# Kernel tuning notes

Hardware: AMD Instinct MI355X
Metric: run time of the kernel (lower is better)

Reference implementation:

```python
import jax, jax.numpy as jnp
import numpy as np
import math

MODEL_DIM = 1024
NUM_HEADS = 16
ATTN_DIM = MODEL_DIM // NUM_HEADS  # 64
ROWS, COLS, AXES = 32, 32, 2
PAIRS = ATTN_DIM // (AXES * 2)     # 16
BATCH = 4
TOKENS = ROWS * COLS               # 1024


def setup_inputs() -> dict:
    key = jax.random.key(0)
    ks = jax.random.split(key, 8)
    s = 1.0 / math.sqrt(MODEL_DIM)
    return {
        "x": jax.random.normal(ks[0], (BATCH, TOKENS, MODEL_DIM), jnp.float32),
        "cos": jax.random.uniform(ks[1], (ROWS, COLS, AXES, PAIRS), jnp.float32),
        "sin": jax.random.uniform(ks[2], (ROWS, COLS, AXES, PAIRS), jnp.float32),
        "Wq": jax.random.normal(ks[3], (MODEL_DIM, MODEL_DIM), jnp.float32) * s,
        "Wk": jax.random.normal(ks[4], (MODEL_DIM, MODEL_DIM), jnp.float32) * s,
        "Wv": jax.random.normal(ks[5], (MODEL_DIM, MODEL_DIM), jnp.float32) * s,
        "Wo": jax.random.normal(ks[6], (MODEL_DIM, MODEL_DIM), jnp.float32) * s,
        "bo": jax.random.normal(ks[7], (MODEL_DIM,), jnp.float32) * 0.01,
    }


def _apply_rope(W, cos, sin):
    # W: (b, h, tokens, attn_dim) -> (b, h, rows, cols, axes, pairs, 2)
    b, h, n, d = W.shape
    rows, cols, axes, pairs = cos.shape
    Wp = W.reshape(b, h, rows, cols, axes, pairs, 2)
    c = cos[None, None]
    s = sin[None, None]
    w0, w1 = Wp[..., 0], Wp[..., 1]
    out = jnp.stack([c * w0 - s * w1, s * w0 + c * w1], axis=-1)
    return out.reshape(b, h, n, d)


def reference(x, cos, sin, Wq, Wk, Wv, Wo, bo):
    b, n, _ = x.shape
    # torch Linear: y = x @ W.T
    Q = (x @ Wq.T).reshape(b, n, NUM_HEADS, ATTN_DIM).transpose(0, 2, 1, 3)
    K = (x @ Wk.T).reshape(b, n, NUM_HEADS, ATTN_DIM).transpose(0, 2, 1, 3)
    V = (x @ Wv.T).reshape(b, n, NUM_HEADS, ATTN_DIM).transpose(0, 2, 1, 3)
    Q = _apply_rope(Q, cos, sin)
    K = _apply_rope(K, cos, sin)
    scores = jnp.einsum("bhqd,bhkd->bhqk", Q, K) / math.sqrt(ATTN_DIM)
    attn = jax.nn.softmax(scores, axis=-1)
    o = jnp.einsum("bhqk,bhkd->bhqd", attn, V)
    o = o.transpose(0, 2, 1, 3).reshape(b, n, MODEL_DIM)
    return o @ Wo.T + bo
```

## Files before the change

kernel.cpp:

```cpp
#include <hip/hip_runtime.h>
#include <hip/hip_bf16.h>

typedef __bf16 bf16;
typedef __bf16 bf16x4 __attribute__((ext_vector_type(4)));
typedef __bf16 bf16x8 __attribute__((ext_vector_type(8)));
typedef float  f32x4  __attribute__((ext_vector_type(4)));
typedef unsigned int u32x2 __attribute__((ext_vector_type(2)));

#define MFMA16(a, b, c) __builtin_amdgcn_mfma_f32_16x16x32_bf16((a), (b), (c), 0, 0, 0)

#define GLOBAL_AS(p) ((const __attribute__((address_space(1))) void*)(p))
#define LDS_AS(p)    ((__attribute__((address_space(3))) void*)(p))

#define BATCH 4
#define TOK   1024
#define DIM   1024
#define HEADS 16
#define HD    64
#define MTOT  (BATCH * TOK)
#define MELEM (1024u * 1024u)

__global__ __launch_bounds__(256) void k_prep(
    const float* __restrict__ X,
    const float* __restrict__ W0, const float* __restrict__ W1,
    const float* __restrict__ W2, const float* __restrict__ W3,
    bf16* __restrict__ xh, bf16* __restrict__ wsp)
{
    const int bid = blockIdx.x;
    if (bid < 2048) {
        size_t i0 = ((size_t)bid * 256 + threadIdx.x) * 8;
        f32x4 a = *(const f32x4*)(X + i0);
        f32x4 b = *(const f32x4*)(X + i0 + 4);
        bf16x8 h;
        #pragma unroll
        for (int j = 0; j < 4; j++) { h[j] = (bf16)a[j]; h[4 + j] = (bf16)b[j]; }
        *(bf16x8*)(xh + i0) = h;
    } else {
        const int b2 = bid - 2048;
        const int widx = b2 >> 9;
        const int inner = b2 & 511;
        const float* W = (widx == 0) ? W0 : (widx == 1) ? W1 : (widx == 2) ? W2 : W3;
        size_t i0 = ((size_t)inner * 256 + threadIdx.x) * 8;
        f32x4 a = *(const f32x4*)(W + i0);
        f32x4 b = *(const f32x4*)(W + i0 + 4);
        bf16x8 h, l;
        #pragma unroll
        for (int j = 0; j < 4; j++) {
            bf16 g0 = (bf16)a[j]; h[j] = g0;     l[j] = (bf16)(a[j] - (float)g0);
            bf16 g1 = (bf16)b[j]; h[4 + j] = g1; l[4 + j] = (bf16)(b[j] - (float)g1);
        }
        *(bf16x8*)(wsp + (size_t)widx * MELEM + i0) = h;
        if (widx == 3)
            *(bf16x8*)(wsp + 4 * (size_t)MELEM + i0) = l;
    }
}

__global__ __launch_bounds__(512) void k_gemmQKV(
    const bf16* __restrict__ Ag, const bf16* __restrict__ wsp,
    const float* __restrict__ cosT, const float* __restrict__ sinT,
    bf16* __restrict__ q_o, bf16* __restrict__ k_o, bf16* __restrict__ v_o)
{
    __shared__ bf16 lds[24576];
    bf16* A0 = lds;
    bf16* A1 = lds + 4096;
    bf16* B0 = lds + 8192;
    bf16* B1 = lds + 16384;

    const int fid = blockIdx.x;
    const int swz = (fid & 7) * 48 + (fid >> 3);
    const int nt = swz % 12;
    const int mt = swz / 12;

    const int t = threadIdx.x;
    const int lane = t & 63;
    const int w = t >> 6;
    const int wr = w >> 2, wc = w & 3;
    const int l15 = lane & 15;
    const int grp = lane >> 4;

    f32x4 acc[4][4];
    #pragma unroll
    for (int m = 0; m < 4; m++)
        #pragma unroll
        for (int n = 0; n < 4; n++)
            #pragma unroll
            for (int r = 0; r < 4; r++) acc[m][n][r] = 0.f;

    const int srow = lane >> 2;
    const int schk8 = ((lane & 3) ^ ((lane >> 3) & 3)) * 8;
    const bf16* asrc = Ag  + (size_t)(mt * 128 + srow) * DIM + schk8;
    const bf16* bsrc = wsp + (size_t)(nt * 256 + srow) * DIM + schk8;

    auto stage = [&](int k, bf16* ab, bf16* bb) {
        const int k0 = k * 32;
        __builtin_amdgcn_global_load_lds(
            GLOBAL_AS(asrc + (size_t)w * 16 * DIM + k0),
            LDS_AS(ab + w * 512), 16, 0, 0);
        #pragma unroll
        for (int jj = 0; jj < 2; ++jj) {
            int j = w * 2 + jj;
            __builtin_amdgcn_global_load_lds(
                GLOBAL_AS(bsrc + (size_t)j * 16 * DIM + k0),
                LDS_AS(bb + j * 512), 16, 0, 0);
        }
    };

    auto compute = [&](const bf16* ab, const bf16* bb) {
        bf16x8 fb[4];
        #pragma unroll
        for (int n = 0; n < 4; n++) {
            int rb = wc * 64 + n * 16 + l15;
            fb[n] = *(const bf16x8*)&bb[rb * 32 + ((grp ^ ((rb >> 1) & 3)) << 3)];
        }
        __builtin_amdgcn_s_setprio(1);
        #pragma unroll
        for (int m = 0; m < 4; m++) {
            int r = wr * 64 + m * 16 + l15;
            bf16x8 fa = *(const bf16x8*)&ab[r * 32 + ((grp ^ ((r >> 1) & 3)) << 3)];
            #pragma unroll
            for (int n = 0; n < 4; n++)
                acc[m][n] = MFMA16(fa, fb[n], acc[m][n]);
        }
        __builtin_amdgcn_s_setprio(0);
    };

    stage(0, A0, B0);
    #pragma unroll 1
    for (int kk = 0; kk < 16; kk++) {
        __syncthreads();
        stage(2 * kk + 1, A1, B1);
        compute(A0, B0);
        __syncthreads();
        if (kk < 15) stage(2 * kk + 2, A0, B0);
        compute(A1, B1);
    }

    const int mode = nt >> 2;
    const int h = (nt & 3) * 4 + wc;
    if (mode == 2) {
        #pragma unroll
        for (int m = 0; m < 4; m++) {
            const int grow0 = mt * 128 + wr * 64 + m * 16 + grp * 4;
            const int b = grow0 >> 10, ntok0 = grow0 & (TOK - 1);
            #pragma unroll
            for (int n = 0; n < 4; n++) {
                const int d = n * 16 + l15;
                bf16x4 pk;
                #pragma unroll
                for (int r = 0; r < 4; r++) pk[r] = (bf16)acc[m][n][r];
                *(bf16x4*)&v_o[((size_t)((b * HEADS + h) * HD + d)) * TOK + ntok0] = pk;
            }
        }
    } else {
        __syncthreads();
        float* cosL = (float*)lds;
        float* sinL = (float*)(lds + 8192);
        const int tb = (mt & 7) * 128;
        *(f32x4*)(cosL + t * 8)     = *(const f32x4*)(cosT + (size_t)tb * 32 + t * 8);
        *(f32x4*)(cosL + t * 8 + 4) = *(const f32x4*)(cosT + (size_t)tb * 32 + t * 8 + 4);
        *(f32x4*)(sinL + t * 8)     = *(const f32x4*)(sinT + (size_t)tb * 32 + t * 8);
        *(f32x4*)(sinL + t * 8 + 4) = *(const f32x4*)(sinT + (size_t)tb * 32 + t * 8 + 4);
        __syncthreads();

        bf16* dst = (mode == 0) ? q_o : k_o;
        const float sc = (mode == 0) ? 0.18033688f : 1.0f;
        #pragma unroll
        for (int m = 0; m < 4; m++) {
            const int grow0 = mt * 128 + wr * 64 + m * 16 + grp * 4;
            const int b = grow0 >> 10, ntok0 = grow0 & (TOK - 1);
            const int loc0 = wr * 64 + m * 16 + grp * 4;
            #pragma unroll
            for (int n = 0; n < 4; n++) {
                const int d = n * 16 + l15;
                const int idp = (d >> 5) * 16 + ((d >> 1) & 15);
                const bool ev = (d & 1) == 0;
                #pragma unroll
                for (int r = 0; r < 4; r++) {
                    float v = acc[m][n][r];
                    float pr = __shfl_xor(v, 1, 64);
                    float c = cosL[(loc0 + r) * 32 + idp];
                    float s = sinL[(loc0 + r) * 32 + idp];
                    float res = (ev ? (c * v - s * pr) : (s * pr + c * v)) * sc;
                    dst[((size_t)(b * HEADS + h) * TOK + ntok0 + r) * HD + d] = (bf16)res;
                }
            }
        }
    }
}

__global__ __launch_bounds__(256) void k_gemmO(
    const bf16* __restrict__ Ag, const bf16* __restrict__ wsp,
    const float* __restrict__ bo, float* __restrict__ f_o)
{
    __shared__ bf16 Alin[64 * 64];
    __shared__ bf16 Bhlin[128 * 64];
    __shared__ bf16 Bllin[128 * 64];

    const bf16* Bh_g = wsp + 3 * (size_t)MELEM;
    const bf16* Bl_g = wsp + 4 * (size_t)MELEM;

    const int fid = blockIdx.x;
    const int swz = (fid & 7) * 64 + (fid >> 3);
    const int nt = swz & 7;
    const int mt = swz >> 3;

    const int t = threadIdx.x;
    const int lane = t & 63;
    const int w = t >> 6;
    const int wr = w >> 1, wc = w & 1;
    const int l15 = lane & 15;

    f32x4 acc[2][4];
    #pragma unroll
    for (int m = 0; m < 2; m++)
        #pragma unroll
        for (int n = 0; n < 4; n++)
            #pragma unroll
            for (int r = 0; r < 4; r++) acc[m][n][r] = 0.f;

    const int srow = lane >> 3;
    const int schk8 = ((lane & 7) ^ (srow & 7)) * 8;
    const bf16* asrc  = Ag   + (size_t)(mt * 64 + srow) * DIM + schk8;
    const bf16* bhsrc = Bh_g + (size_t)(nt * 128 + srow) * DIM + schk8;
    const bf16* blsrc = Bl_g + (size_t)(nt * 128 + srow) * DIM + schk8;

    for (int k0 = 0; k0 < DIM; k0 += 64) {
        __syncthreads();
        #pragma unroll
        for (int ii = 0; ii < 2; ++ii) {
            int i = w * 2 + ii;
            __builtin_amdgcn_global_load_lds(
                GLOBAL_AS(asrc + (size_t)i * 8 * DIM + k0),
                LDS_AS(&Alin[i * 512]), 16, 0, 0);
        }
        #pragma unroll
        for (int jj = 0; jj < 4; ++jj) {
            int j = w * 4 + jj;
            size_t roff = (size_t)j * 8 * DIM + k0;
            __builtin_amdgcn_global_load_lds(GLOBAL_AS(bhsrc + roff),
                                             LDS_AS(&Bhlin[j * 512]), 16, 0, 0);
            __builtin_amdgcn_global_load_lds(GLOBAL_AS(blsrc + roff),
                                             LDS_AS(&Bllin[j * 512]), 16, 0, 0);
        }
        __syncthreads();

        #pragma unroll
        for (int ks = 0; ks < 2; ks++) {
            const int cc = (lane >> 4) + ks * 4;
            bf16x8 fbh[4], fbl[4];
            #pragma unroll
            for (int n = 0; n < 4; n++) {
                int r = wc * 64 + n * 16 + l15;
                int off = r * 64 + ((cc ^ (r & 7)) << 3);
                fbh[n] = *(const bf16x8*)&Bhlin[off];
                fbl[n] = *(const bf16x8*)&Bllin[off];
            }
            #pragma unroll
            for (int m = 0; m < 2; m++) {
                int r = wr * 32 + m * 16 + l15;
                bf16x8 fa = *(const bf16x8*)&Alin[r * 64 + ((cc ^ (r & 7)) << 3)];
                #pragma unroll
                for (int n = 0; n < 4; n++) {
                    acc[m][n] = MFMA16(fa, fbh[n], acc[m][n]);
                    acc[m][n] = MFMA16(fa, fbl[n], acc[m][n]);
                }
            }
        }
    }

    #pragma unroll
    for (int m = 0; m < 2; m++) {
        #pragma unroll
        for (int n = 0; n < 4; n++) {
            const int grow0 = mt * 64 + wr * 32 + m * 16 + (lane >> 4) * 4;
            const int gcol  = nt * 128 + wc * 64 + n * 16 + l15;
            const float bias = bo[gcol];
            #pragma unroll
            for (int r = 0; r < 4; r++)
                f_o[(size_t)(grow0 + r) * DIM + gcol] = acc[m][n][r] + bias;
        }
    }
}

__global__ __launch_bounds__(256) void k_attn(
    const bf16* __restrict__ Q, const bf16* __restrict__ K,
    const bf16* __restrict__ Vt, bf16* __restrict__ O)
{
    __shared__ bf16 Ks0[64 * 64];
    __shared__ bf16 Ks1[64 * 64];
    __shared__ bf16 Vs0[64 * 64];
    __shared__ bf16 Vs1[64 * 64];
    __shared__ bf16 Ps[64 * 64];

    const int fid = blockIdx.x;
    const int swz = (fid & 7) * 128 + (fid >> 3);
    const int qt = swz & 15;
    const int bh = swz >> 4;

    const int t = threadIdx.x;
    const int lane = t & 63;
    const int w = t >> 6;
    const int col = lane & 15;
    const int grp = lane >> 4;
    const int m7 = col & 7;
    const int qrow = w * 16 + col;

    const bf16* qp = Q + ((size_t)bh * TOK + qt * 64 + qrow) * HD + grp * 8;
    bf16x8 qf0 = *(const bf16x8*)qp;
    bf16x8 qf1 = *(const bf16x8*)(qp + 32);

    const int srow = lane >> 3;
    const int schk8 = ((lane & 7) ^ (srow & 7)) * 8;
    const bf16* ksrc = K  + ((size_t)bh * TOK + srow) * HD + schk8;
    const bf16* vsrc = Vt + ((size_t)bh * HD + srow) * TOK + schk8;

    bf16x8 ones;
    #pragma unroll
    for (int j = 0; j < 8; j++) ones[j] = (bf16)1.0f;

    f32x4 zero = {0.f, 0.f, 0.f, 0.f};
    f32x4 lacc = zero;
    f32x4 o_[4];
    #pragma unroll
    for (int dt = 0; dt < 4; dt++) o_[dt] = zero;

    unsigned int* PsU = (unsigned int*)Ps;

    auto stage = [&](int kt, bf16* kb, bf16* vb) {
        #pragma unroll
        for (int ii = 0; ii < 2; ++ii) {
            int i = w * 2 + ii;
            __builtin_amdgcn_global_load_lds(
                GLOBAL_AS(ksrc + (size_t)(kt * 64 + i * 8) * HD),
                LDS_AS(kb + i * 512), 16, 0, 0);
            __builtin_amdgcn_global_load_lds(
                GLOBAL_AS(vsrc + (size_t)(i * 8) * TOK + kt * 64),
                LDS_AS(vb + i * 512), 16, 0, 0);
        }
    };

    auto compute = [&](const bf16* kb, const bf16* vb) {
        f32x4 s[4];
        #pragma unroll
        for (int ct = 0; ct < 4; ct++) s[ct] = zero;
        __builtin_amdgcn_s_setprio(1);
        #pragma unroll
        for (int ct = 0; ct < 4; ct++) {
            int rbase = (ct * 16 + col) * 64;
            bf16x8 kf0 = *(const bf16x8*)&kb[rbase + ((grp ^ m7) << 3)];
            bf16x8 kf1 = *(const bf16x8*)&kb[rbase + (((grp + 4) ^ m7) << 3)];
            s[ct] = MFMA16(kf0, qf0, s[ct]);
            s[ct] = MFMA16(kf1, qf1, s[ct]);
        }
        __builtin_amdgcn_s_setprio(0);

        #pragma unroll
        for (int ct = 0; ct < 4; ct++) {
            float p0 = exp2f(s[ct][0]);
            float p1 = exp2f(s[ct][1]);
            float p2 = exp2f(s[ct][2]);
            float p3 = exp2f(s[ct][3]);
            unsigned int a0, a1;
            asm("v_cvt_pk_bf16_f32 %0, %1, %2" : "=v"(a0) : "v"(p0), "v"(p1));
            asm("v_cvt_pk_bf16_f32 %0, %1, %2" : "=v"(a1) : "v"(p2), "v"(p3));
            int cs = (2 * ct + (grp >> 1)) ^ m7;
            u32x2 st = {a0, a1};
            *(u32x2*)&PsU[qrow * 32 + cs * 4 + (grp & 1) * 2] = st;
        }

        __builtin_amdgcn_s_setprio(1);
        #pragma unroll
        for (int tt = 0; tt < 2; tt++) {
            const int coff = ((4 * tt + grp) ^ m7) << 3;
            bf16x8 pf = *(const bf16x8*)&Ps[qrow * 64 + coff];
            lacc = MFMA16(ones, pf, lacc);
            #pragma unroll
            for (int dt = 0; dt < 4; dt++) {
                bf16x8 vf = *(const bf16x8*)&vb[(dt * 16 + col) * 64 + coff];
                o_[dt] = MFMA16(vf, pf, o_[dt]);
            }
        }
        __builtin_amdgcn_s_setprio(0);
    };

    stage(0, Ks0, Vs0);
    #pragma unroll 1
    for (int kk = 0; kk < 8; kk++) {
        __syncthreads();
        stage(2 * kk + 1, Ks1, Vs1);
        compute(Ks0, Vs0);
        __syncthreads();
        if (kk < 7) stage(2 * kk + 2, Ks0, Vs0);
        compute(Ks1, Vs1);
    }

    const float inv = 1.0f / lacc[0];

    const int b = bh >> 4, h = bh & 15;
    const int ntok = qt * 64 + qrow;
    #pragma unroll
    for (int dt = 0; dt < 4; dt++) {
        bf16x4 pk4;
        #pragma unroll
        for (int r = 0; r < 4; r++) pk4[r] = (bf16)(o_[dt][r] * inv);
        *(bf16x4*)&O[((size_t)b * TOK + ntok) * DIM + h * HD + dt * 16 + grp * 4] = pk4;
    }
}

extern "C" void kernel_launch(void* const* d_in, const int* in_sizes, int n_in,
                              void* d_out, int out_size, void* d_ws, size_t ws_size,
                              hipStream_t stream)
{
    const float* x    = (const float*)d_in[0];
    const float* cosT = (const float*)d_in[1];
    const float* sinT = (const float*)d_in[2];
    const float* Wq   = (const float*)d_in[3];
    const float* Wk   = (const float*)d_in[4];
    const float* Wv   = (const float*)d_in[5];
    const float* Wo   = (const float*)d_in[6];
    const float* bo   = (const float*)d_in[7];
    float* out = (float*)d_out;

    bf16* xh  = (bf16*)d_ws;
    bf16* qw  = xh + 4 * (size_t)MELEM;
    bf16* kw  = qw + 4 * (size_t)MELEM;
    bf16* vw  = kw + 4 * (size_t)MELEM;
    bf16* wsp = vw + 4 * (size_t)MELEM;
    bf16* ow  = xh;

    k_prep<<<dim3(4096), dim3(256), 0, stream>>>(x, Wq, Wk, Wv, Wo, xh, wsp);
    k_gemmQKV<<<dim3(384), dim3(512), 0, stream>>>(xh, wsp, cosT, sinT, qw, kw, vw);
    k_attn<<<dim3(1024), dim3(256), 0, stream>>>(qw, kw, vw, ow);
    k_gemmO<<<dim3(512), dim3(256), 0, stream>>>(ow, wsp, bo, out);
}
```

Baseline: 99.79 us.

## Process two 64-row query tiles per attention block to reuse K/V tiles

Each attention workgroup now handles 128 query rows as two 64-row sub-tiles sharing the same staged K and V LDS tiles, halving the grid to 512 blocks. This halves the K/V global-to-LDS traffic per query row and amortises the staging and barriers over twice the MFMA work. In exchange the kernel uses more registers (two sets of accumulators and Q fragments) and LDS for a doubled P buffer, and with fewer blocks occupancy and latency hiding may drop.

```diff
diff --git a/kernel.cpp b/kernel.cpp
--- a/kernel.cpp
+++ b/kernel.cpp
@@ -290,12 +290,12 @@
     __shared__ bf16 Ks1[64 * 64];
     __shared__ bf16 Vs0[64 * 64];
     __shared__ bf16 Vs1[64 * 64];
-    __shared__ bf16 Ps[64 * 64];
+    __shared__ bf16 Ps[128 * 64];
 
     const int fid = blockIdx.x;
-    const int swz = (fid & 7) * 128 + (fid >> 3);
-    const int qt = swz & 15;
-    const int bh = swz >> 4;
+    const int swz = (fid & 7) * 64 + (fid >> 3);
+    const int qt = swz & 7;
+    const int bh = swz >> 3;
 
     const int t = threadIdx.x;
     const int lane = t & 63;
@@ -305,9 +305,11 @@
     const int m7 = col & 7;
     const int qrow = w * 16 + col;
 
-    const bf16* qp = Q + ((size_t)bh * TOK + qt * 64 + qrow) * HD + grp * 8;
-    bf16x8 qf0 = *(const bf16x8*)qp;
-    bf16x8 qf1 = *(const bf16x8*)(qp + 32);
+    const bf16* qp = Q + ((size_t)bh * TOK + qt * 128 + qrow) * HD + grp * 8;
+    bf16x8 qa0 = *(const bf16x8*)qp;
+    bf16x8 qb0 = *(const bf16x8*)(qp + 32);
+    bf16x8 qa1 = *(const bf16x8*)(qp + (size_t)64 * HD);
+    bf16x8 qb1 = *(const bf16x8*)(qp + (size_t)64 * HD + 32);
 
     const int srow = lane >> 3;
     const int schk8 = ((lane & 7) ^ (srow & 7)) * 8;
@@ -319,10 +321,10 @@
     for (int j = 0; j < 8; j++) ones[j] = (bf16)1.0f;
 
     f32x4 zero = {0.f, 0.f, 0.f, 0.f};
-    f32x4 lacc = zero;
-    f32x4 o_[4];
-    #pragma unroll
-    for (int dt = 0; dt < 4; dt++) o_[dt] = zero;
+    f32x4 laccA = zero, laccB = zero;
+    f32x4 oA[4], oB[4];
+    #pragma unroll
+    for (int dt = 0; dt < 4; dt++) { oA[dt] = zero; oB[dt] = zero; }
 
     unsigned int* PsU = (unsigned int*)Ps;
 
@@ -340,44 +342,62 @@
     };
 
     auto compute = [&](const bf16* kb, const bf16* vb) {
-        f32x4 s[4];
-        #pragma unroll
-        for (int ct = 0; ct < 4; ct++) s[ct] = zero;
+        f32x4 s0[4], s1[4];
+        #pragma unroll
+        for (int ct = 0; ct < 4; ct++) { s0[ct] = zero; s1[ct] = zero; }
         __builtin_amdgcn_s_setprio(1);
         #pragma unroll
         for (int ct = 0; ct < 4; ct++) {
             int rbase = (ct * 16 + col) * 64;
             bf16x8 kf0 = *(const bf16x8*)&kb[rbase + ((grp ^ m7) << 3)];
             bf16x8 kf1 = *(const bf16x8*)&kb[rbase + (((grp + 4) ^ m7) << 3)];
-            s[ct] = MFMA16(kf0, qf0, s[ct]);
-            s[ct] = MFMA16(kf1, qf1, s[ct]);
+            s0[ct] = MFMA16(kf0, qa0, s0[ct]);
+            s0[ct] = MFMA16(kf1, qb0, s0[ct]);
+            s1[ct] = MFMA16(kf0, qa1, s1[ct]);
+            s1[ct] = MFMA16(kf1, qb1, s1[ct]);
         }
         __builtin_amdgcn_s_setprio(0);
 
         #pragma unroll
         for (int ct = 0; ct < 4; ct++) {
-            float p0 = exp2f(s[ct][0]);
-            float p1 = exp2f(s[ct][1]);
-            float p2 = exp2f(s[ct][2]);
-            float p3 = exp2f(s[ct][3]);
-            unsigned int a0, a1;
-            asm("v_cvt_pk_bf16_f32 %0, %1, %2" : "=v"(a0) : "v"(p0), "v"(p1));
-            asm("v_cvt_pk_bf16_f32 %0, %1, %2" : "=v"(a1) : "v"(p2), "v"(p3));
             int cs = (2 * ct + (grp >> 1)) ^ m7;
-            u32x2 st = {a0, a1};
-            *(u32x2*)&PsU[qrow * 32 + cs * 4 + (grp & 1) * 2] = st;
+            {
+                float p0 = exp2f(s0[ct][0]);
+                float p1 = exp2f(s0[ct][1]);
+                float p2 = exp2f(s0[ct][2]);
+                float p3 = exp2f(s0[ct][3]);
+                unsigned int a0, a1;
+                asm("v_cvt_pk_bf16_f32 %0, %1, %2" : "=v"(a0) : "v"(p0), "v"(p1));
+                asm("v_cvt_pk_bf16_f32 %0, %1, %2" : "=v"(a1) : "v"(p2), "v"(p3));
+                u32x2 st = {a0, a1};
+                *(u32x2*)&PsU[qrow * 32 + cs * 4 + (grp & 1) * 2] = st;
+            }
+            {
+                float p0 = exp2f(s1[ct][0]);
+                float p1 = exp2f(s1[ct][1]);
+                float p2 = exp2f(s1[ct][2]);
+                float p3 = exp2f(s1[ct][3]);
+                unsigned int a0, a1;
+                asm("v_cvt_pk_bf16_f32 %0, %1, %2" : "=v"(a0) : "v"(p0), "v"(p1));
+                asm("v_cvt_pk_bf16_f32 %0, %1, %2" : "=v"(a1) : "v"(p2), "v"(p3));
+                u32x2 st = {a0, a1};
+                *(u32x2*)&PsU[(64 + qrow) * 32 + cs * 4 + (grp & 1) * 2] = st;
+            }
         }
 
         __builtin_amdgcn_s_setprio(1);
         #pragma unroll
         for (int tt = 0; tt < 2; tt++) {
             const int coff = ((4 * tt + grp) ^ m7) << 3;
-            bf16x8 pf = *(const bf16x8*)&Ps[qrow * 64 + coff];
-            lacc = MFMA16(ones, pf, lacc);
+            bf16x8 pfA = *(const bf16x8*)&Ps[qrow * 64 + coff];
+            bf16x8 pfB = *(const bf16x8*)&Ps[(64 + qrow) * 64 + coff];
+            laccA = MFMA16(ones, pfA, laccA);
+            laccB = MFMA16(ones, pfB, laccB);
             #pragma unroll
             for (int dt = 0; dt < 4; dt++) {
                 bf16x8 vf = *(const bf16x8*)&vb[(dt * 16 + col) * 64 + coff];
-                o_[dt] = MFMA16(vf, pf, o_[dt]);
+                oA[dt] = MFMA16(vf, pfA, oA[dt]);
+                oB[dt] = MFMA16(vf, pfB, oB[dt]);
             }
         }
         __builtin_amdgcn_s_setprio(0);
@@ -394,16 +414,21 @@
         compute(Ks1, Vs1);
     }
 
-    const float inv = 1.0f / lacc[0];
+    const float invA = 1.0f / laccA[0];
+    const float invB = 1.0f / laccB[0];
 
     const int b = bh >> 4, h = bh & 15;
-    const int ntok = qt * 64 + qrow;
+    const int nt0 = qt * 128 + qrow;
     #pragma unroll
     for (int dt = 0; dt < 4; dt++) {
-        bf16x4 pk4;
-        #pragma unroll
-        for (int r = 0; r < 4; r++) pk4[r] = (bf16)(o_[dt][r] * inv);
-        *(bf16x4*)&O[((size_t)b * TOK + ntok) * DIM + h * HD + dt * 16 + grp * 4] = pk4;
+        bf16x4 pkA, pkB;
+        #pragma unroll
+        for (int r = 0; r < 4; r++) {
+            pkA[r] = (bf16)(oA[dt][r] * invA);
+            pkB[r] = (bf16)(oB[dt][r] * invB);
+        }
+        *(bf16x4*)&O[((size_t)b * TOK + nt0) * DIM + h * HD + dt * 16 + grp * 4] = pkA;
+        *(bf16x4*)&O[((size_t)b * TOK + nt0 + 64) * DIM + h * HD + dt * 16 + grp * 4] = pkB;
     }
 }
 
@@ -430,6 +455,6 @@
 
     k_prep<<<dim3(4096), dim3(256), 0, stream>>>(x, Wq, Wk, Wv, Wo, xh, wsp);
     k_gemmQKV<<<dim3(384), dim3(512), 0, stream>>>(xh, wsp, cosT, sinT, qw, kw, vw);
-    k_attn<<<dim3(1024), dim3(256), 0, stream>>>(qw, kw, vw, ow);
+    k_attn<<<dim3(512), dim3(256), 0, stream>>>(qw, kw, vw, ow);
     k_gemmO<<<dim3(512), dim3(256), 0, stream>>>(ow, wsp, bo, out);
 }
```

Measured after the change: 98.62 us. About the same (-1.2%).

## Software-pipeline attention loop so QK^T overlaps previous tile's softmax and PV

Applied to the files above, without the earlier changes.

Splits K and V staging and separates the QK^T MFMA phase from the exp/pack/PV phase. The loop now computes scores for the current key tile while running exp and PV for the previous tile, with V loads issued one step later. The goal is to hide the latency of the exp and LDS round-trip behind independent MFMA work and to separate the K and V transfers. In exchange it keeps a second set of score registers live, which may raise VGPR pressure, and it adds an epilogue step after the loop.

```diff
diff --git a/kernel.cpp b/kernel.cpp
--- a/kernel.cpp
+++ b/kernel.cpp
@@ -326,21 +326,26 @@
 
     unsigned int* PsU = (unsigned int*)Ps;
 
-    auto stage = [&](int kt, bf16* kb, bf16* vb) {
+    auto stageK = [&](int kt, bf16* kb) {
         #pragma unroll
         for (int ii = 0; ii < 2; ++ii) {
             int i = w * 2 + ii;
             __builtin_amdgcn_global_load_lds(
                 GLOBAL_AS(ksrc + (size_t)(kt * 64 + i * 8) * HD),
                 LDS_AS(kb + i * 512), 16, 0, 0);
+        }
+    };
+    auto stageV = [&](int kt, bf16* vb) {
+        #pragma unroll
+        for (int ii = 0; ii < 2; ++ii) {
+            int i = w * 2 + ii;
             __builtin_amdgcn_global_load_lds(
                 GLOBAL_AS(vsrc + (size_t)(i * 8) * TOK + kt * 64),
                 LDS_AS(vb + i * 512), 16, 0, 0);
         }
     };
 
-    auto compute = [&](const bf16* kb, const bf16* vb) {
-        f32x4 s[4];
+    auto qkt = [&](const bf16* kb, f32x4* s) {
         #pragma unroll
         for (int ct = 0; ct < 4; ct++) s[ct] = zero;
         __builtin_amdgcn_s_setprio(1);
@@ -353,7 +358,9 @@
             s[ct] = MFMA16(kf1, qf1, s[ct]);
         }
         __builtin_amdgcn_s_setprio(0);
-
+    };
+
+    auto packpv = [&](const f32x4* s, const bf16* vb) {
         #pragma unroll
         for (int ct = 0; ct < 4; ct++) {
             float p0 = exp2f(s[ct][0]);
@@ -367,7 +374,6 @@
             u32x2 st = {a0, a1};
             *(u32x2*)&PsU[qrow * 32 + cs * 4 + (grp & 1) * 2] = st;
         }
-
         __builtin_amdgcn_s_setprio(1);
         #pragma unroll
         for (int tt = 0; tt < 2; tt++) {
@@ -383,16 +389,25 @@
         __builtin_amdgcn_s_setprio(0);
     };
 
-    stage(0, Ks0, Vs0);
+    f32x4 sa[4], sprev[4];
+
+    stageK(0, Ks0);
+    stageV(0, Vs0);
     #pragma unroll 1
     for (int kk = 0; kk < 8; kk++) {
         __syncthreads();
-        stage(2 * kk + 1, Ks1, Vs1);
-        compute(Ks0, Vs0);
-        __syncthreads();
-        if (kk < 7) stage(2 * kk + 2, Ks0, Vs0);
-        compute(Ks1, Vs1);
-    }
+        stageK(2 * kk + 1, Ks1);
+        if (kk > 0) stageV(2 * kk, Vs0);
+        qkt(Ks0, sa);
+        if (kk > 0) packpv(sprev, Vs1);
+        __syncthreads();
+        if (kk < 7) stageK(2 * kk + 2, Ks0);
+        stageV(2 * kk + 1, Vs1);
+        qkt(Ks1, sprev);
+        packpv(sa, Vs0);
+    }
+    __syncthreads();
+    packpv(sprev, Vs1);
 
     const float inv = 1.0f / lacc[0];
 
```

Result: no change. 98.92 us (median of 2 runs) (-0.9%).
